# Kernel tuning notes

Measured on AMD Instinct MI355X. Metric: run time of the kernel, lower is better.

Reference implementation:

```python
import jax, jax.numpy as jnp
import numpy as np

B, T, C = 2, 2048, 2048
H, KV, DH = 32, 8, 64
GROUP = H // KV  # 4


def _rope_tables(seq_len, half_dim):
    # standard RoPE frequencies: theta_i = 10000^(-2i/d)
    inv_freq = 1.0 / (10000.0 ** (np.arange(half_dim, dtype=np.float32) * 2.0 / (2 * half_dim)))
    ang = np.arange(seq_len, dtype=np.float32)[:, None] * inv_freq[None, :]  # [T, D/2]
    return jnp.asarray(np.sin(ang)), jnp.asarray(np.cos(ang))


def setup_inputs() -> dict:
    key = jax.random.key(0)
    ks = jax.random.split(key, 5)
    scale = 0.02
    sin, cos = _rope_tables(T, DH // 2)
    return {
        "x": jax.random.normal(ks[0], (B, T, C), jnp.float32),
        "Wq": jax.random.normal(ks[1], (C, H * DH), jnp.float32) * scale,
        "Wk": jax.random.normal(ks[2], (C, KV * DH), jnp.float32) * scale,
        "Wv": jax.random.normal(ks[3], (C, KV * DH), jnp.float32) * scale,
        "Wout": jax.random.normal(ks[4], (H * DH, C), jnp.float32) * scale,
        "rope_sin": sin,
        "rope_cos": cos,
        "swa_window": 2048,
    }


def apply_rope(x, sin, cos):
    # x: [B, T, Hh, D]; interleaved-pair rotation, computed in fp32
    b, t, h, d = x.shape
    orig_dtype = x.dtype
    xf = x.astype(jnp.float32).reshape(b, t, h, d // 2, 2)
    x1, x2 = xf[..., 0], xf[..., 1]
    s = sin[:t].astype(jnp.float32)[None, :, None, :]  # [1,T,1,D/2]
    c = cos[:t].astype(jnp.float32)[None, :, None, :]
    o1 = x1 * c - x2 * s
    o2 = x1 * s + x2 * c
    return jnp.stack([o1, o2], axis=-1).reshape(b, t, h, d).astype(orig_dtype)


def reference(x, Wq, Wk, Wv, Wout, rope_sin, rope_cos, swa_window):
    b, t, c = x.shape
    q = (x @ Wq).reshape(b, t, H, DH)
    k = (x @ Wk).reshape(b, t, KV, DH)
    v = (x @ Wv).reshape(b, t, KV, DH)
    q = apply_rope(q, rope_sin, rope_cos)
    k = apply_rope(k, rope_sin, rope_cos)
    # expand KV heads (repeat_interleave along head dim)
    k_e = jnp.repeat(k, GROUP, axis=2)  # [B,T,H,DH]
    v_e = jnp.repeat(v, GROUP, axis=2)
    scale = 1.0 / jnp.sqrt(jnp.float32(DH))
    scores = jnp.einsum('bqhd,bkhd->bhqk', q, k_e) * scale  # [B,H,T,T]
    idx = jnp.arange(t)
    causal_mask = idx[None, :] > idx[:, None]                 # j > i
    older = (idx[:, None] - idx[None, :]) > swa_window        # beyond window
    mask = causal_mask | older
    scores = jnp.where(mask[None, None], -jnp.inf, scores)
    weights = jax.nn.softmax(scores, axis=-1)
    attn = jnp.einsum('bhqk,bkhd->bqhd', weights, v_e).reshape(b, t, c)
    return attn @ Wout
```

## Files before the change

### kernel.cpp

```cpp
#include <hip/hip_runtime.h>

typedef unsigned short u16;
typedef unsigned int u32;
typedef __attribute__((ext_vector_type(8))) short bf16x8;
typedef __attribute__((ext_vector_type(4))) float f32x4;

#define B_   2
#define T_   2048
#define C_   2048
#define H_   32
#define KVH_ 8
#define DH_  64
#define QKVS 3072
#define KOFF 2048
#define VOFF 2560

__device__ __forceinline__ u16 f2bf(float f) {
  union { float f; unsigned u; } v; v.f = f;
  unsigned r = (v.u + 0x7fffu + ((v.u >> 16) & 1u)) >> 16;
  return (u16)r;
}
__device__ __forceinline__ float bf2f(u16 u) {
  union { unsigned u; float f; } v; v.u = ((unsigned)u) << 16;
  return v.f;
}
__device__ __forceinline__ u32 cvt_pk_bf16(float lo, float hi) {
  u32 r;
  asm("v_cvt_pk_bf16_f32 %0, %1, %2" : "=v"(r) : "v"(lo), "v"(hi));
  return r;
}
__device__ __forceinline__ void async_copy16(void* lds, const void* g) {
  __builtin_amdgcn_global_load_lds((const __attribute__((address_space(1))) void*)g,
                                   (__attribute__((address_space(3))) void*)lds, 16, 0, 0);
}

__global__ void cvt_bf16_kernel(const float* __restrict__ in, u16* __restrict__ out, int n4) {
  int i = blockIdx.x * 256 + threadIdx.x;
  if (i >= n4) return;
  const float4 v = reinterpret_cast<const float4*>(in)[i];
  union { u16 h[4]; unsigned long long ll; } o;
  o.h[0] = f2bf(v.x); o.h[1] = f2bf(v.y); o.h[2] = f2bf(v.z); o.h[3] = f2bf(v.w);
  reinterpret_cast<unsigned long long*>(out)[i] = o.ll;
}

__global__ void transpose_w_kernel(const float* __restrict__ W, u16* __restrict__ Wt,
                                   int K_, int N_) {
  __shared__ float tile[32][33];
  int n0 = blockIdx.x * 32, k0 = blockIdx.y * 32;
  int tx = threadIdx.x, ty = threadIdx.y;
#pragma unroll
  for (int i = 0; i < 4; i++)
    tile[ty + i * 8][tx] = W[(long)(k0 + ty + i * 8) * N_ + n0 + tx];
  __syncthreads();
#pragma unroll
  for (int i = 0; i < 4; i++)
    Wt[(long)(n0 + ty + i * 8) * K_ + k0 + tx] = f2bf(tile[tx][ty + i * 8]);
}

__global__ void rope_kernel(u16* __restrict__ buf, const float* __restrict__ sT,
                            const float* __restrict__ cT, int rowstride, int ncols) {
  int row = blockIdx.y;
  int c4 = (blockIdx.x * 128 + threadIdx.x) * 4;
  if (c4 >= ncols) return;
  const float S = (blockIdx.x < 4) ? 0.18033688f : 1.0f;
  int t = row & (T_ - 1);
  int pair = (c4 & (DH_ - 1)) >> 1;
  u16* p = buf + (long)row * rowstride + c4;
  union { u16 h[4]; unsigned long long ll; } v;
  v.ll = *reinterpret_cast<unsigned long long*>(p);
  float x0 = bf2f(v.h[0]), x1 = bf2f(v.h[1]), x2 = bf2f(v.h[2]), x3 = bf2f(v.h[3]);
  float s0 = sT[t * 32 + pair] * S,     c0 = cT[t * 32 + pair] * S;
  float s1 = sT[t * 32 + pair + 1] * S, c1 = cT[t * 32 + pair + 1] * S;
  v.h[0] = f2bf(x0 * c0 - x1 * s0);
  v.h[1] = f2bf(x0 * s0 + x1 * c0);
  v.h[2] = f2bf(x2 * c1 - x3 * s1);
  v.h[3] = f2bf(x2 * s1 + x3 * c1);
  *reinterpret_cast<unsigned long long*>(p) = v.ll;
}

template <int OUT_F32>
__global__ __launch_bounds__(256, 3) void gemm_nt(const u16* __restrict__ A,
                                                  const u16* __restrict__ Bt,
                                                  void* __restrict__ Cout,
                                                  int M_, int N_, int K_) {
  __shared__ alignas(16) u16 As[128 * 32];
  __shared__ alignas(16) u16 Bs[128 * 32];
  const int t = threadIdx.x;
  const int w = t >> 6, l = t & 63;
  const int gx = gridDim.x;
  const int nwg = gx * gridDim.y;
  const int flat = blockIdx.y * gx + blockIdx.x;
  const int f2 = (flat & 7) * (nwg >> 3) + (flat >> 3);
  const int m0 = (f2 / gx) * 128, n0 = (f2 % gx) * 128;
  const int wr = (w >> 1) * 64, wc = (w & 1) * 64;
  const int lr = l & 15, lk = (l >> 4) * 8;

  f32x4 acc[4][4];
#pragma unroll
  for (int i = 0; i < 4; i++)
#pragma unroll
    for (int j = 0; j < 4; j++) {
      f32x4 z = {0.f, 0.f, 0.f, 0.f};
      acc[i][j] = z;
    }

  const int arow = t >> 2, acol = (t & 3) * 8;
  const u16* Ag = A + (long)(m0 + arow) * K_ + acol;
  const u16* Bg = Bt + (long)(n0 + arow) * K_ + acol;
  char* AsB = (char*)As;
  char* BsB = (char*)Bs;
  const int ldsbase = (w << 10);

  for (int kt = 0; kt < K_; kt += 32) {
    async_copy16(AsB + ldsbase, Ag + kt);
    async_copy16(AsB + 4096 + ldsbase, Ag + (long)64 * K_ + kt);
    async_copy16(BsB + ldsbase, Bg + kt);
    async_copy16(BsB + 4096 + ldsbase, Bg + (long)64 * K_ + kt);
    __syncthreads();
    bf16x8 a[4], b[4];
#pragma unroll
    for (int i = 0; i < 4; i++) a[i] = *(const bf16x8*)(As + (wr + i * 16 + lr) * 32 + lk);
#pragma unroll
    for (int i = 0; i < 4; i++) b[i] = *(const bf16x8*)(Bs + (wc + i * 16 + lr) * 32 + lk);
#pragma unroll
    for (int i = 0; i < 4; i++)
#pragma unroll
      for (int j = 0; j < 4; j++)
        acc[i][j] = __builtin_amdgcn_mfma_f32_16x16x32_bf16(a[i], b[j], acc[i][j], 0, 0, 0);
    __syncthreads();
  }

  const int lg = l >> 4;
#pragma unroll
  for (int i = 0; i < 4; i++)
#pragma unroll
    for (int j = 0; j < 4; j++)
#pragma unroll
      for (int r = 0; r < 4; r++) {
        long row = m0 + wr + i * 16 + lg * 4 + r;
        long col = n0 + wc + j * 16 + lr;
        float v = acc[i][j][r];
        if (OUT_F32)
          ((float*)Cout)[row * N_ + col] = v;
        else
          ((u16*)Cout)[row * N_ + col] = f2bf(v);
      }
}

__global__ __launch_bounds__(256, 3) void attn_fwd(const u16* __restrict__ qkv,
                                                   u16* __restrict__ o,
                                                   const int* __restrict__ swa_ptr) {
  __shared__ alignas(16) u16 Klds[64 * 64];
  __shared__ alignas(16) u16 VTlds[64 * 64];
  __shared__ alignas(16) u16 Plds[4][16 * 64];
  const int t = threadIdx.x, w = t >> 6, l = t & 63;
  const int flat = blockIdx.x + (blockIdx.y << 4) + (blockIdx.z << 9);
  const int f2 = (flat & 7) * 128 + (flat >> 3);
  const int bx = f2 & 15, h = (f2 >> 4) & 31, b = f2 >> 9;
  const int kvh = h >> 2;
  const int swa = *swa_ptr;
  const int lr = l & 15, lg = l >> 4;
  const int swz = (lr & 7) << 4;
  const int sbase = (l & 48) | (lg << 2);
  char* myP = (char*)Plds + w * 2048;

  const int krow = t >> 3, kch = t & 7;
  const int kvp = (t & 31) * 2, dch = (t >> 5) * 8;

  for (int pass = 0; pass < 2; pass++) {
    const int qtile = pass ? (31 - bx) : bx;
    const int q0 = qtile * 64;

    bf16x8 qa[2];
    const long qrow = (long)(b * T_ + q0 + w * 16 + lr);
#pragma unroll
    for (int kk = 0; kk < 2; kk++)
      qa[kk] = *(const bf16x8*)(qkv + qrow * QKVS + h * 64 + kk * 32 + lg * 8);

    f32x4 ofrag[4];
#pragma unroll
    for (int nf = 0; nf < 4; nf++) {
      f32x4 z = {0.f, 0.f, 0.f, 0.f};
      ofrag[nf] = z;
    }
    float mrun = -1e30f, srun = 0.f;

    const int lo = q0 - swa - 63;
    const int startt = lo > 0 ? ((lo + 63) >> 6) : 0;

    bf16x8 K0, K1, V0, V1;
    {
      const u16* kbase = qkv + (long)(b * T_ + startt * 64) * QKVS + KOFF + kvh * 64;
      K0 = *(const bf16x8*)(kbase + (long)krow * QKVS + kch * 8);
      K1 = *(const bf16x8*)(kbase + (long)(krow + 32) * QKVS + kch * 8);
      const u16* vbase = qkv + (long)(b * T_ + startt * 64) * QKVS + VOFF + kvh * 64 + dch;
      V0 = *(const bf16x8*)(vbase + (long)kvp * QKVS);
      V1 = *(const bf16x8*)(vbase + (long)(kvp + 1) * QKVS);
    }

    for (int tt = startt; tt <= qtile; tt++) {
      const int kv0 = tt * 64;
      __syncthreads();
      *(bf16x8*)((char*)Klds + ((krow * 128 + kch * 16) ^ ((krow & 7) << 4))) = K0;
      *(bf16x8*)((char*)Klds + (((krow + 32) * 128 + kch * 16) ^ ((krow & 7) << 4))) = K1;
#pragma unroll
      for (int i = 0; i < 8; i++) {
        int d = dch + i;
        int off = (d * 128 + kvp * 2) ^ ((d & 7) << 4);
        u32 pack = ((u32)(u16)V0[i]) | (((u32)(u16)V1[i]) << 16);
        *(u32*)((char*)VTlds + off) = pack;
      }
      __syncthreads();
      if (tt < qtile) {
        const u16* kbase = qkv + (long)(b * T_ + kv0 + 64) * QKVS + KOFF + kvh * 64;
        K0 = *(const bf16x8*)(kbase + (long)krow * QKVS + kch * 8);
        K1 = *(const bf16x8*)(kbase + (long)(krow + 32) * QKVS + kch * 8);
        const u16* vbase = qkv + (long)(b * T_ + kv0 + 64) * QKVS + VOFF + kvh * 64 + dch;
        V0 = *(const bf16x8*)(vbase + (long)kvp * QKVS);
        V1 = *(const bf16x8*)(vbase + (long)(kvp + 1) * QKVS);
      }

      f32x4 s[4];
#pragma unroll
      for (int nf = 0; nf < 4; nf++) {
        f32x4 acc = {0.f, 0.f, 0.f, 0.f};
#pragma unroll
        for (int kk = 0; kk < 2; kk++) {
          int koff = ((nf * 16 + lr) * 128 + (kk * 32 + lg * 8) * 2) ^ swz;
          bf16x8 kb = *(const bf16x8*)((char*)Klds + koff);
          acc = __builtin_amdgcn_mfma_f32_16x16x32_bf16(kb, qa[kk], acc, 0, 0, 0);
        }
        s[nf] = acc;
      }

      const int i_abs = q0 + w * 16 + lr;
      const int wmin = q0 + w * 16;
      float pm = -3e38f;
      if ((kv0 + 63 > wmin) || (wmin + 15 - kv0 > swa)) {
#pragma unroll
        for (int nf = 0; nf < 4; nf++)
#pragma unroll
          for (int r = 0; r < 4; r++) {
            int j = kv0 + nf * 16 + lg * 4 + r;
            bool ok = (j <= i_abs) && (i_abs - j <= swa);
            float sv = ok ? s[nf][r] : -3e38f;
            s[nf][r] = sv;
            pm = fmaxf(pm, sv);
          }
      } else {
#pragma unroll
        for (int nf = 0; nf < 4; nf++)
#pragma unroll
          for (int r = 0; r < 4; r++) pm = fmaxf(pm, s[nf][r]);
      }
      pm = fmaxf(pm, __shfl_xor(pm, 16));
      pm = fmaxf(pm, __shfl_xor(pm, 32));

      float mnew = fmaxf(mrun, pm);
      float fac = exp2f(mrun - mnew);
      mrun = mnew;
      float rs = 0.f;
#pragma unroll
      for (int nf = 0; nf < 4; nf++)
#pragma unroll
        for (int r = 0; r < 4; r++) {
          float p = exp2f(s[nf][r] - mrun);
          s[nf][r] = p;
          rs += p;
        }
      rs += __shfl_xor(rs, 16);
      rs += __shfl_xor(rs, 32);
      srun = srun * fac + rs;

#pragma unroll
      for (int nf = 0; nf < 4; nf++) {
        u32 lo32 = cvt_pk_bf16(s[nf][0], s[nf][1]);
        u32 hi32 = cvt_pk_bf16(s[nf][2], s[nf][3]);
        unsigned long long pk = ((unsigned long long)hi32 << 32) | lo32;
        int off = (lr * 128 + nf * 32 + lg * 8) ^ swz;
        *(unsigned long long*)(myP + off) = pk;
      }

      float facr[4];
#pragma unroll
      for (int r = 0; r < 4; r++) facr[r] = __shfl(fac, sbase + r);
#pragma unroll
      for (int nf = 0; nf < 4; nf++)
#pragma unroll
        for (int r = 0; r < 4; r++) ofrag[nf][r] *= facr[r];

      asm volatile("s_waitcnt lgkmcnt(0)" ::: "memory");
      bf16x8 pa[2];
#pragma unroll
      for (int kk = 0; kk < 2; kk++) {
        int poff = (lr * 128 + kk * 64 + lg * 16) ^ swz;
        pa[kk] = *(const bf16x8*)(myP + poff);
      }
#pragma unroll
      for (int nf = 0; nf < 4; nf++)
#pragma unroll
        for (int kk = 0; kk < 2; kk++) {
          int voff = ((nf * 16 + lr) * 128 + (kk * 32 + lg * 8) * 2) ^ swz;
          bf16x8 vb = *(const bf16x8*)((char*)VTlds + voff);
          ofrag[nf] = __builtin_amdgcn_mfma_f32_16x16x32_bf16(pa[kk], vb, ofrag[nf], 0, 0, 0);
        }
    }

    float inv = 1.0f / srun;
    float invr[4];
#pragma unroll
    for (int r = 0; r < 4; r++) invr[r] = __shfl(inv, sbase + r);
    const long orow = (long)(b * T_ + q0 + w * 16);
#pragma unroll
    for (int nf = 0; nf < 4; nf++)
#pragma unroll
      for (int r = 0; r < 4; r++)
        o[(orow + lg * 4 + r) * 2048 + h * 64 + nf * 16 + lr] = f2bf(ofrag[nf][r] * invr[r]);
  }
}

extern "C" void kernel_launch(void* const* d_in, const int* in_sizes, int n_in,
                              void* d_out, int out_size, void* d_ws, size_t ws_size,
                              hipStream_t stream) {
  const float* x    = (const float*)d_in[0];
  const float* Wq   = (const float*)d_in[1];
  const float* Wk   = (const float*)d_in[2];
  const float* Wv   = (const float*)d_in[3];
  const float* Wout = (const float*)d_in[4];
  const float* rsin = (const float*)d_in[5];
  const float* rcos = (const float*)d_in[6];
  const int*   swa  = (const int*)d_in[7];
  float* out = (float*)d_out;

  char* ws = (char*)d_ws;
  u16* xb    = (u16*)(ws);
  u16* ab    = xb;
  u16* wqkvT = (u16*)(ws + 16777216);
  u16* woT   = wqkvT;
  u16* qkvb  = (u16*)(ws + 29360128);

  cvt_bf16_kernel<<<dim3(8192), dim3(256), 0, stream>>>(x, xb, 2097152);
  transpose_w_kernel<<<dim3(64, 64), dim3(32, 8), 0, stream>>>(Wq, wqkvT, 2048, 2048);
  transpose_w_kernel<<<dim3(16, 64), dim3(32, 8), 0, stream>>>(Wk, wqkvT + (long)2048 * 2048, 2048, 512);
  transpose_w_kernel<<<dim3(16, 64), dim3(32, 8), 0, stream>>>(Wv, wqkvT + (long)2560 * 2048, 2048, 512);

  gemm_nt<0><<<dim3(24, 32), dim3(256), 0, stream>>>(xb, wqkvT, qkvb, 4096, 3072, 2048);

  transpose_w_kernel<<<dim3(64, 64), dim3(32, 8), 0, stream>>>(Wout, woT, 2048, 2048);

  rope_kernel<<<dim3(5, 4096), dim3(128), 0, stream>>>(qkvb, rsin, rcos, QKVS, 2560);

  attn_fwd<<<dim3(16, 32, 2), dim3(256), 0, stream>>>(qkvb, ab, swa);

  gemm_nt<1><<<dim3(16, 32), dim3(256), 0, stream>>>(ab, woT, out, 4096, 2048, 2048);
}
```

Measured before the change: 333.4 us.

## Double K-tile depth in GEMM and KV tile size in attention

```diff
diff --git a/kernel.cpp b/kernel.cpp
--- a/kernel.cpp
+++ b/kernel.cpp
@@ -83,8 +83,8 @@
                                                   const u16* __restrict__ Bt,
                                                   void* __restrict__ Cout,
                                                   int M_, int N_, int K_) {
-  __shared__ alignas(16) u16 As[128 * 32];
-  __shared__ alignas(16) u16 Bs[128 * 32];
+  __shared__ alignas(16) u16 As[128 * 64];
+  __shared__ alignas(16) u16 Bs[128 * 64];
   const int t = threadIdx.x;
   const int w = t >> 6, l = t & 63;
   const int gx = gridDim.x;
@@ -93,7 +93,8 @@
   const int f2 = (flat & 7) * (nwg >> 3) + (flat >> 3);
   const int m0 = (f2 / gx) * 128, n0 = (f2 % gx) * 128;
   const int wr = (w >> 1) * 64, wc = (w & 1) * 64;
-  const int lr = l & 15, lk = (l >> 4) * 8;
+  const int lr = l & 15, lg = l >> 4;
+  const int rswz = (lr & 7) << 4;
 
   f32x4 acc[4][4];
 #pragma unroll
@@ -104,33 +105,39 @@
       acc[i][j] = z;
     }
 
-  const int arow = t >> 2, acol = (t & 3) * 8;
-  const u16* Ag = A + (long)(m0 + arow) * K_ + acol;
-  const u16* Bg = Bt + (long)(n0 + arow) * K_ + acol;
+  const int arow = t >> 3;
+  const int achk = (t & 7) ^ (arow & 7);
+  const u16* Ag = A + (long)(m0 + arow) * K_ + achk * 8;
+  const u16* Bg = Bt + (long)(n0 + arow) * K_ + achk * 8;
   char* AsB = (char*)As;
   char* BsB = (char*)Bs;
-  const int ldsbase = (w << 10);
-
-  for (int kt = 0; kt < K_; kt += 32) {
-    async_copy16(AsB + ldsbase, Ag + kt);
-    async_copy16(AsB + 4096 + ldsbase, Ag + (long)64 * K_ + kt);
-    async_copy16(BsB + ldsbase, Bg + kt);
-    async_copy16(BsB + 4096 + ldsbase, Bg + (long)64 * K_ + kt);
+  const int wbase = (w << 10);
+
+  for (int kt = 0; kt < K_; kt += 64) {
+#pragma unroll
+    for (int r = 0; r < 4; r++) {
+      async_copy16(AsB + r * 4096 + wbase, Ag + kt + (long)(32 * r) * K_);
+      async_copy16(BsB + r * 4096 + wbase, Bg + kt + (long)(32 * r) * K_);
+    }
     __syncthreads();
-    bf16x8 a[4], b[4];
-#pragma unroll
-    for (int i = 0; i < 4; i++) a[i] = *(const bf16x8*)(As + (wr + i * 16 + lr) * 32 + lk);
-#pragma unroll
-    for (int i = 0; i < 4; i++) b[i] = *(const bf16x8*)(Bs + (wc + i * 16 + lr) * 32 + lk);
-#pragma unroll
-    for (int i = 0; i < 4; i++)
-#pragma unroll
-      for (int j = 0; j < 4; j++)
-        acc[i][j] = __builtin_amdgcn_mfma_f32_16x16x32_bf16(a[i], b[j], acc[i][j], 0, 0, 0);
+#pragma unroll
+    for (int kk = 0; kk < 2; kk++) {
+      bf16x8 a[4], b[4];
+#pragma unroll
+      for (int i = 0; i < 4; i++)
+        a[i] = *(const bf16x8*)(AsB + (wr + i * 16 + lr) * 128 + ((kk * 64 + lg * 16) ^ rswz));
+#pragma unroll
+      for (int i = 0; i < 4; i++)
+        b[i] = *(const bf16x8*)(BsB + (wc + i * 16 + lr) * 128 + ((kk * 64 + lg * 16) ^ rswz));
+#pragma unroll
+      for (int i = 0; i < 4; i++)
+#pragma unroll
+        for (int j = 0; j < 4; j++)
+          acc[i][j] = __builtin_amdgcn_mfma_f32_16x16x32_bf16(a[i], b[j], acc[i][j], 0, 0, 0);
+    }
     __syncthreads();
   }
 
-  const int lg = l >> 4;
 #pragma unroll
   for (int i = 0; i < 4; i++)
 #pragma unroll
@@ -150,8 +157,8 @@
 __global__ __launch_bounds__(256, 3) void attn_fwd(const u16* __restrict__ qkv,
                                                    u16* __restrict__ o,
                                                    const int* __restrict__ swa_ptr) {
-  __shared__ alignas(16) u16 Klds[64 * 64];
-  __shared__ alignas(16) u16 VTlds[64 * 64];
+  __shared__ alignas(16) u16 Klds[128 * 64];
+  __shared__ alignas(16) u16 VTlds[64 * 128];
   __shared__ alignas(16) u16 Plds[4][16 * 64];
   const int t = threadIdx.x, w = t >> 6, l = t & 63;
   const int flat = blockIdx.x + (blockIdx.y << 4) + (blockIdx.z << 9);
@@ -165,7 +172,7 @@
   char* myP = (char*)Plds + w * 2048;
 
   const int krow = t >> 3, kch = t & 7;
-  const int kvp = (t & 31) * 2, dch = (t >> 5) * 8;
+  const int kvp = (t & 63) * 2, dch = (t >> 6) * 8;
 
   for (int pass = 0; pass < 2; pass++) {
     const int qtile = pass ? (31 - bx) : bx;
@@ -185,44 +192,58 @@
     }
     float mrun = -1e30f, srun = 0.f;
 
-    const int lo = q0 - swa - 63;
-    const int startt = lo > 0 ? ((lo + 63) >> 6) : 0;
-
-    bf16x8 K0, K1, V0, V1;
+    const int lastt = qtile >> 1;
+    const int lo = q0 - swa;
+    const int startt = lo > 0 ? (lo >> 7) : 0;
+
+    bf16x8 K0, K1, K2, K3, Va0, Va1, Vb0, Vb1;
     {
-      const u16* kbase = qkv + (long)(b * T_ + startt * 64) * QKVS + KOFF + kvh * 64;
-      K0 = *(const bf16x8*)(kbase + (long)krow * QKVS + kch * 8);
-      K1 = *(const bf16x8*)(kbase + (long)(krow + 32) * QKVS + kch * 8);
-      const u16* vbase = qkv + (long)(b * T_ + startt * 64) * QKVS + VOFF + kvh * 64 + dch;
-      V0 = *(const bf16x8*)(vbase + (long)kvp * QKVS);
-      V1 = *(const bf16x8*)(vbase + (long)(kvp + 1) * QKVS);
-    }
-
-    for (int tt = startt; tt <= qtile; tt++) {
-      const int kv0 = tt * 64;
+      const u16* kb = qkv + (long)(b * T_ + startt * 128) * QKVS + KOFF + kvh * 64;
+      K0 = *(const bf16x8*)(kb + (long)krow * QKVS + kch * 8);
+      K1 = *(const bf16x8*)(kb + (long)(krow + 32) * QKVS + kch * 8);
+      K2 = *(const bf16x8*)(kb + (long)(krow + 64) * QKVS + kch * 8);
+      K3 = *(const bf16x8*)(kb + (long)(krow + 96) * QKVS + kch * 8);
+      const u16* vb = qkv + (long)(b * T_ + startt * 128) * QKVS + VOFF + kvh * 64;
+      Va0 = *(const bf16x8*)(vb + (long)kvp * QKVS + dch);
+      Va1 = *(const bf16x8*)(vb + (long)(kvp + 1) * QKVS + dch);
+      Vb0 = *(const bf16x8*)(vb + (long)kvp * QKVS + dch + 32);
+      Vb1 = *(const bf16x8*)(vb + (long)(kvp + 1) * QKVS + dch + 32);
+    }
+
+    for (int tt = startt; tt <= lastt; tt++) {
+      const int kv0 = tt * 128;
       __syncthreads();
-      *(bf16x8*)((char*)Klds + ((krow * 128 + kch * 16) ^ ((krow & 7) << 4))) = K0;
-      *(bf16x8*)((char*)Klds + (((krow + 32) * 128 + kch * 16) ^ ((krow & 7) << 4))) = K1;
+      const int kkey = (krow & 7) << 4;
+      *(bf16x8*)((char*)Klds + ((krow * 128 + kch * 16) ^ kkey)) = K0;
+      *(bf16x8*)((char*)Klds + (((krow + 32) * 128 + kch * 16) ^ kkey)) = K1;
+      *(bf16x8*)((char*)Klds + (((krow + 64) * 128 + kch * 16) ^ kkey)) = K2;
+      *(bf16x8*)((char*)Klds + (((krow + 96) * 128 + kch * 16) ^ kkey)) = K3;
 #pragma unroll
       for (int i = 0; i < 8; i++) {
         int d = dch + i;
-        int off = (d * 128 + kvp * 2) ^ ((d & 7) << 4);
-        u32 pack = ((u32)(u16)V0[i]) | (((u32)(u16)V1[i]) << 16);
-        *(u32*)((char*)VTlds + off) = pack;
+        int off = (d * 256 + kvp * 2) ^ ((i & 7) << 4);
+        *(u32*)((char*)VTlds + off) = ((u32)(u16)Va0[i]) | (((u32)(u16)Va1[i]) << 16);
+        int d2 = d + 32;
+        int off2 = (d2 * 256 + kvp * 2) ^ ((i & 7) << 4);
+        *(u32*)((char*)VTlds + off2) = ((u32)(u16)Vb0[i]) | (((u32)(u16)Vb1[i]) << 16);
       }
       __syncthreads();
-      if (tt < qtile) {
-        const u16* kbase = qkv + (long)(b * T_ + kv0 + 64) * QKVS + KOFF + kvh * 64;
-        K0 = *(const bf16x8*)(kbase + (long)krow * QKVS + kch * 8);
-        K1 = *(const bf16x8*)(kbase + (long)(krow + 32) * QKVS + kch * 8);
-        const u16* vbase = qkv + (long)(b * T_ + kv0 + 64) * QKVS + VOFF + kvh * 64 + dch;
-        V0 = *(const bf16x8*)(vbase + (long)kvp * QKVS);
-        V1 = *(const bf16x8*)(vbase + (long)(kvp + 1) * QKVS);
-      }
-
-      f32x4 s[4];
-#pragma unroll
-      for (int nf = 0; nf < 4; nf++) {
+      if (tt < lastt) {
+        const u16* kb = qkv + (long)(b * T_ + kv0 + 128) * QKVS + KOFF + kvh * 64;
+        K0 = *(const bf16x8*)(kb + (long)krow * QKVS + kch * 8);
+        K1 = *(const bf16x8*)(kb + (long)(krow + 32) * QKVS + kch * 8);
+        K2 = *(const bf16x8*)(kb + (long)(krow + 64) * QKVS + kch * 8);
+        K3 = *(const bf16x8*)(kb + (long)(krow + 96) * QKVS + kch * 8);
+        const u16* vb = qkv + (long)(b * T_ + kv0 + 128) * QKVS + VOFF + kvh * 64;
+        Va0 = *(const bf16x8*)(vb + (long)kvp * QKVS + dch);
+        Va1 = *(const bf16x8*)(vb + (long)(kvp + 1) * QKVS + dch);
+        Vb0 = *(const bf16x8*)(vb + (long)kvp * QKVS + dch + 32);
+        Vb1 = *(const bf16x8*)(vb + (long)(kvp + 1) * QKVS + dch + 32);
+      }
+
+      f32x4 s[8];
+#pragma unroll
+      for (int nf = 0; nf < 8; nf++) {
         f32x4 acc = {0.f, 0.f, 0.f, 0.f};
 #pragma unroll
         for (int kk = 0; kk < 2; kk++) {
@@ -236,9 +257,9 @@
       const int i_abs = q0 + w * 16 + lr;
       const int wmin = q0 + w * 16;
       float pm = -3e38f;
-      if ((kv0 + 63 > wmin) || (wmin + 15 - kv0 > swa)) {
-#pragma unroll
-        for (int nf = 0; nf < 4; nf++)
+      if ((kv0 + 127 > wmin) || (wmin + 15 - kv0 > swa)) {
+#pragma unroll
+        for (int nf = 0; nf < 8; nf++)
 #pragma unroll
           for (int r = 0; r < 4; r++) {
             int j = kv0 + nf * 16 + lg * 4 + r;
@@ -249,7 +270,7 @@
           }
       } else {
 #pragma unroll
-        for (int nf = 0; nf < 4; nf++)
+        for (int nf = 0; nf < 8; nf++)
 #pragma unroll
           for (int r = 0; r < 4; r++) pm = fmaxf(pm, s[nf][r]);
       }
@@ -261,7 +282,7 @@
       mrun = mnew;
       float rs = 0.f;
 #pragma unroll
-      for (int nf = 0; nf < 4; nf++)
+      for (int nf = 0; nf < 8; nf++)
 #pragma unroll
         for (int r = 0; r < 4; r++) {
           float p = exp2f(s[nf][r] - mrun);
@@ -273,37 +294,41 @@
       srun = srun * fac + rs;
 
 #pragma unroll
-      for (int nf = 0; nf < 4; nf++) {
-        u32 lo32 = cvt_pk_bf16(s[nf][0], s[nf][1]);
-        u32 hi32 = cvt_pk_bf16(s[nf][2], s[nf][3]);
-        unsigned long long pk = ((unsigned long long)hi32 << 32) | lo32;
-        int off = (lr * 128 + nf * 32 + lg * 8) ^ swz;
-        *(unsigned long long*)(myP + off) = pk;
-      }
-
-      float facr[4];
-#pragma unroll
-      for (int r = 0; r < 4; r++) facr[r] = __shfl(fac, sbase + r);
-#pragma unroll
-      for (int nf = 0; nf < 4; nf++)
-#pragma unroll
-        for (int r = 0; r < 4; r++) ofrag[nf][r] *= facr[r];
-
-      asm volatile("s_waitcnt lgkmcnt(0)" ::: "memory");
-      bf16x8 pa[2];
-#pragma unroll
-      for (int kk = 0; kk < 2; kk++) {
-        int poff = (lr * 128 + kk * 64 + lg * 16) ^ swz;
-        pa[kk] = *(const bf16x8*)(myP + poff);
-      }
-#pragma unroll
-      for (int nf = 0; nf < 4; nf++)
+      for (int hh = 0; hh < 2; hh++) {
+#pragma unroll
+        for (int n2 = 0; n2 < 4; n2++) {
+          int nf = hh * 4 + n2;
+          u32 lo32 = cvt_pk_bf16(s[nf][0], s[nf][1]);
+          u32 hi32 = cvt_pk_bf16(s[nf][2], s[nf][3]);
+          unsigned long long pk = ((unsigned long long)hi32 << 32) | lo32;
+          int off = (lr * 128 + n2 * 32 + lg * 8) ^ swz;
+          *(unsigned long long*)(myP + off) = pk;
+        }
+        if (hh == 0) {
+          float facr[4];
+#pragma unroll
+          for (int r = 0; r < 4; r++) facr[r] = __shfl(fac, sbase + r);
+#pragma unroll
+          for (int nf = 0; nf < 4; nf++)
+#pragma unroll
+            for (int r = 0; r < 4; r++) ofrag[nf][r] *= facr[r];
+        }
+        asm volatile("s_waitcnt lgkmcnt(0)" ::: "memory");
+        bf16x8 pa[2];
 #pragma unroll
         for (int kk = 0; kk < 2; kk++) {
-          int voff = ((nf * 16 + lr) * 128 + (kk * 32 + lg * 8) * 2) ^ swz;
-          bf16x8 vb = *(const bf16x8*)((char*)VTlds + voff);
-          ofrag[nf] = __builtin_amdgcn_mfma_f32_16x16x32_bf16(pa[kk], vb, ofrag[nf], 0, 0, 0);
-        }
+          int poff = (lr * 128 + kk * 64 + lg * 16) ^ swz;
+          pa[kk] = *(const bf16x8*)(myP + poff);
+        }
+#pragma unroll
+        for (int nf = 0; nf < 4; nf++)
+#pragma unroll
+          for (int kk = 0; kk < 2; kk++) {
+            int voff = ((nf * 16 + lr) * 256 + (hh * 64 + kk * 32 + lg * 8) * 2) ^ swz;
+            bf16x8 vb = *(const bf16x8*)((char*)VTlds + voff);
+            ofrag[nf] = __builtin_amdgcn_mfma_f32_16x16x32_bf16(pa[kk], vb, ofrag[nf], 0, 0, 0);
+          }
+      }
     }
 
     float inv = 1.0f / srun;
```

New measurement: 363.7 us. 9.1% more time.
